# Performance work log

Measured on AMD Instinct MI355X. Metric: run time of the kernel, lower is better.

## Reference

```python
import jax, jax.numpy as jnp
import numpy as np

LOSS_WEIGHT = 20.0

def setup_inputs() -> dict:
    key = jax.random.key(0)
    ks = jax.random.split(key, 6)
    b, f, ns, nb, h, w = 8, 4, 7, 7, 128, 128
    # BCE input: keep strictly inside (0,1)
    segmentations = jax.random.uniform(ks[0], (b, f, nb, h, w), jnp.float32, 1e-4, 1.0 - 1e-4)
    masks = jax.random.uniform(ks[1], (b, f, ns, h, w), jnp.float32)
    reconstructions = jax.random.uniform(ks[2], (b, f, nb, 3, h, w), jnp.float32)
    rec_tgt = jax.random.uniform(ks[3], (b, f, 3, h, w), jnp.float32)
    masks_vis = jax.random.uniform(ks[4], (b, f, ns, h, w), jnp.float32)
    attn_index = jax.random.uniform(ks[5], (b, f, ns, nb), jnp.float32)
    return dict(segmentations=segmentations, masks=masks, reconstructions=reconstructions,
                rec_tgt=rec_tgt, masks_vis=masks_vis, attn_index=attn_index)

def reference(segmentations, masks, reconstructions, rec_tgt, masks_vis, attn_index):
    b, f, nb, h, w = segmentations.shape
    ns = masks.shape[2]
    N = b * f
    # broadcast instead of repeat: seg -> [N,1,nb,h,w], masks -> [N,ns,1,h,w]
    seg = segmentations.reshape(N, 1, nb, h, w)
    m = (masks.reshape(N, ns, 1, h, w) > 0.5).astype(seg.dtype)
    # torch BCE clamps log terms at -100
    logp = jnp.clip(jnp.log(seg), -100.0)
    log1mp = jnp.clip(jnp.log(1.0 - seg), -100.0)
    bce = -(m * logp + (1.0 - m) * log1mp)
    bce_term = jnp.sum(bce, axis=(-1, -2)) / (h * w)  # [N, ns, nb]
    # visibility mask broadcast over buffer and channel dims
    mv = (masks_vis.reshape(N, ns, 1, 1, h, w) > 0.5).astype(seg.dtype)
    rec_pred = reconstructions.reshape(N, 1, nb, 3, h, w) * mv   # [N,ns,nb,3,h,w]
    tgt = rec_tgt.reshape(N, 1, 1, 3, h, w) * mv
    mse_term = jnp.sum((rec_pred - tgt) ** 2, axis=(-3, -2, -1))  # [N, ns, nb]
    loss = bce_term + 0.1 * mse_term
    ai = attn_index.reshape(N, ns, nb)
    total = jnp.sum(ai * loss) / (b * f * ns * nb)
    return total * LOSS_WEIGHT
```

## Files before the change

kernel.cpp:

```cpp
#include <hip/hip_runtime.h>

#define HW 16384
#define NB 7
#define NS 7
#define NN 32

__global__ void zero_out_kernel(float* out) {
    if (threadIdx.x == 0 && blockIdx.x == 0) out[0] = 0.0f;
}

__global__ __launch_bounds__(256) void em_loss_kernel(
    const float* __restrict__ seg,
    const float* __restrict__ masks,
    const float* __restrict__ rec,
    const float* __restrict__ tgt,
    const float* __restrict__ mvis,
    const float* __restrict__ ai,
    float* __restrict__ out)
{
    const int n   = blockIdx.y;
    const int tid = threadIdx.x;
    const int pix = (blockIdx.x * blockDim.x + tid) * 4;

    __shared__ float s_ai[NS * NB];
    __shared__ float s_A[NB];
    __shared__ float s_part[4];

    if (tid < NS * NB) s_ai[tid] = ai[n * NS * NB + tid];
    __syncthreads();
    if (tid < NB) {
        float a = 0.0f;
        #pragma unroll
        for (int s = 0; s < NS; ++s) a += s_ai[s * NB + tid];
        s_A[tid] = a;
    }
    __syncthreads();

    const float* seg_n = seg   + (size_t)n * NB * HW + pix;
    const float* rec_n = rec   + (size_t)n * NB * 3 * HW + pix;
    const float* tgt_n = tgt   + (size_t)n * 3 * HW + pix;
    const float* msk_n = masks + (size_t)n * NS * HW + pix;
    const float* mv_n  = mvis  + (size_t)n * NS * HW + pix;

    float t[3][4];
    #pragma unroll
    for (int c = 0; c < 3; ++c) {
        float4 v = *reinterpret_cast<const float4*>(tgt_n + c * HW);
        t[c][0] = v.x; t[c][1] = v.y; t[c][2] = v.z; t[c][3] = v.w;
    }

    float d2[NB][4];
    #pragma unroll
    for (int b = 0; b < NB; ++b) {
        #pragma unroll
        for (int j = 0; j < 4; ++j) d2[b][j] = 0.0f;
        #pragma unroll
        for (int c = 0; c < 3; ++c) {
            float4 v = *reinterpret_cast<const float4*>(rec_n + (b * 3 + c) * HW);
            float r[4] = {v.x, v.y, v.z, v.w};
            #pragma unroll
            for (int j = 0; j < 4; ++j) {
                float d = r[j] - t[c][j];
                d2[b][j] += d * d;
            }
        }
    }

    float base[4] = {0.f, 0.f, 0.f, 0.f};
    float Ldiff[NB][4];
    #pragma unroll
    for (int b = 0; b < NB; ++b) {
        float4 v = *reinterpret_cast<const float4*>(seg_n + b * HW);
        float sv[4] = {v.x, v.y, v.z, v.w};
        float A = s_A[b];
        #pragma unroll
        for (int j = 0; j < 4; ++j) {
            float L1 = fminf(-__logf(sv[j]), 100.0f);
            float L0 = fminf(-__logf(1.0f - sv[j]), 100.0f);
            base[j] += A * L0;
            Ldiff[b][j] = L1 - L0;
        }
    }

    float bce[4] = {base[0], base[1], base[2], base[3]};
    float mse[4] = {0.f, 0.f, 0.f, 0.f};
    #pragma unroll
    for (int s = 0; s < NS; ++s) {
        float dotL[4] = {0.f, 0.f, 0.f, 0.f};
        float dotD[4] = {0.f, 0.f, 0.f, 0.f};
        #pragma unroll
        for (int b = 0; b < NB; ++b) {
            float a = s_ai[s * NB + b];
            #pragma unroll
            for (int j = 0; j < 4; ++j) {
                dotL[j] += a * Ldiff[b][j];
                dotD[j] += a * d2[b][j];
            }
        }
        float4 mk = *reinterpret_cast<const float4*>(msk_n + s * HW);
        float4 mv = *reinterpret_cast<const float4*>(mv_n + s * HW);
        float mkv[4] = {mk.x, mk.y, mk.z, mk.w};
        float mvv[4] = {mv.x, mv.y, mv.z, mv.w};
        #pragma unroll
        for (int j = 0; j < 4; ++j) {
            bce[j] += (mkv[j] > 0.5f) ? dotL[j] : 0.0f;
            mse[j] += (mvv[j] > 0.5f) ? dotD[j] : 0.0f;
        }
    }

    const float inv_hw = 1.0f / (float)HW;
    float acc = 0.0f;
    #pragma unroll
    for (int j = 0; j < 4; ++j) acc += bce[j] * inv_hw + 0.1f * mse[j];

    #pragma unroll
    for (int off = 32; off > 0; off >>= 1) acc += __shfl_down(acc, off, 64);

    const int wave = tid >> 6;
    const int lane = tid & 63;
    if (lane == 0) s_part[wave] = acc;
    __syncthreads();
    if (tid == 0) {
        float tsum = s_part[0] + s_part[1] + s_part[2] + s_part[3];
        atomicAdd(out, tsum * (20.0f / 1568.0f));
    }
}

extern "C" void kernel_launch(void* const* d_in, const int* in_sizes, int n_in,
                              void* d_out, int out_size, void* d_ws, size_t ws_size,
                              hipStream_t stream) {
    const float* seg  = (const float*)d_in[0];
    const float* msk  = (const float*)d_in[1];
    const float* rec  = (const float*)d_in[2];
    const float* tgt  = (const float*)d_in[3];
    const float* mvis = (const float*)d_in[4];
    const float* ai   = (const float*)d_in[5];
    float* out = (float*)d_out;

    zero_out_kernel<<<1, 64, 0, stream>>>(out);
    dim3 grid(HW / (256 * 4), NN);
    em_loss_kernel<<<grid, 256, 0, stream>>>(seg, msk, rec, tgt, mvis, ai, out);
}
```

Measured before the change: 123.6 us.

## Use one pixel per thread, precompute mask weights, and reduce partials without atomics

Each thread now handles one pixel with scalar loads instead of four pixels with float4, which gives four times as many blocks (2048) to hide memory latency. The per-pixel mask bits are folded into weight vectors over the buffer dimension, which lowers register pressure and avoids holding per-buffer intermediate arrays. The atomic accumulation and the zeroing kernel are replaced by per-block partials written to workspace, followed by a single-block reduction kernel. The cost is narrower loads and one more kernel launch, and the new path relies on the workspace being large enough for the partials.

```diff
diff --git a/kernel.cpp b/kernel.cpp
--- a/kernel.cpp
+++ b/kernel.cpp
@@ -4,23 +4,22 @@
 #define NB 7
 #define NS 7
 #define NN 32
+#define BLK 256
+#define GRIDX (HW / BLK)
+#define NPART (GRIDX * NN)
 
-__global__ void zero_out_kernel(float* out) {
-    if (threadIdx.x == 0 && blockIdx.x == 0) out[0] = 0.0f;
-}
-
-__global__ __launch_bounds__(256) void em_loss_kernel(
+__global__ __launch_bounds__(BLK, 4) void em_loss_main(
     const float* __restrict__ seg,
     const float* __restrict__ masks,
     const float* __restrict__ rec,
     const float* __restrict__ tgt,
     const float* __restrict__ mvis,
     const float* __restrict__ ai,
-    float* __restrict__ out)
+    float* __restrict__ partial)
 {
     const int n   = blockIdx.y;
     const int tid = threadIdx.x;
-    const int pix = (blockIdx.x * blockDim.x + tid) * 4;
+    const int pix = blockIdx.x * BLK + tid;
 
     __shared__ float s_ai[NS * NB];
     __shared__ float s_A[NB];
@@ -42,88 +41,75 @@
     const float* msk_n = masks + (size_t)n * NS * HW + pix;
     const float* mv_n  = mvis  + (size_t)n * NS * HW + pix;
 
-    float t[3][4];
+    float mkv[NS], mvv[NS];
     #pragma unroll
-    for (int c = 0; c < 3; ++c) {
-        float4 v = *reinterpret_cast<const float4*>(tgt_n + c * HW);
-        t[c][0] = v.x; t[c][1] = v.y; t[c][2] = v.z; t[c][3] = v.w;
-    }
+    for (int s = 0; s < NS; ++s) mkv[s] = msk_n[s * HW];
+    #pragma unroll
+    for (int s = 0; s < NS; ++s) mvv[s] = mv_n[s * HW];
 
-    float d2[NB][4];
+    float wl[NB], wd[NB];
     #pragma unroll
-    for (int b = 0; b < NB; ++b) {
+    for (int b = 0; b < NB; ++b) { wl[b] = 0.0f; wd[b] = 0.0f; }
+    #pragma unroll
+    for (int s = 0; s < NS; ++s) {
+        const float bm = (mkv[s] > 0.5f) ? 1.0f : 0.0f;
+        const float bv = (mvv[s] > 0.5f) ? 1.0f : 0.0f;
         #pragma unroll
-        for (int j = 0; j < 4; ++j) d2[b][j] = 0.0f;
-        #pragma unroll
-        for (int c = 0; c < 3; ++c) {
-            float4 v = *reinterpret_cast<const float4*>(rec_n + (b * 3 + c) * HW);
-            float r[4] = {v.x, v.y, v.z, v.w};
-            #pragma unroll
-            for (int j = 0; j < 4; ++j) {
-                float d = r[j] - t[c][j];
-                d2[b][j] += d * d;
-            }
+        for (int b = 0; b < NB; ++b) {
+            const float a = s_ai[s * NB + b];
+            wl[b] += bm * a;
+            wd[b] += bv * a;
         }
     }
 
-    float base[4] = {0.f, 0.f, 0.f, 0.f};
-    float Ldiff[NB][4];
+    const float t0 = tgt_n[0];
+    const float t1 = tgt_n[HW];
+    const float t2 = tgt_n[2 * HW];
+
+    float acc_bce = 0.0f, acc_mse = 0.0f;
     #pragma unroll
     for (int b = 0; b < NB; ++b) {
-        float4 v = *reinterpret_cast<const float4*>(seg_n + b * HW);
-        float sv[4] = {v.x, v.y, v.z, v.w};
-        float A = s_A[b];
-        #pragma unroll
-        for (int j = 0; j < 4; ++j) {
-            float L1 = fminf(-__logf(sv[j]), 100.0f);
-            float L0 = fminf(-__logf(1.0f - sv[j]), 100.0f);
-            base[j] += A * L0;
-            Ldiff[b][j] = L1 - L0;
-        }
+        const float sv = seg_n[b * HW];
+        const float r0 = rec_n[(b * 3 + 0) * HW];
+        const float r1 = rec_n[(b * 3 + 1) * HW];
+        const float r2 = rec_n[(b * 3 + 2) * HW];
+        const float L1 = fminf(-__logf(sv), 100.0f);
+        const float L0 = fminf(-__logf(1.0f - sv), 100.0f);
+        acc_bce += s_A[b] * L0 + wl[b] * (L1 - L0);
+        const float d0 = r0 - t0, d1 = r1 - t1, d2 = r2 - t2;
+        acc_mse += wd[b] * (d0 * d0 + d1 * d1 + d2 * d2);
     }
 
-    float bce[4] = {base[0], base[1], base[2], base[3]};
-    float mse[4] = {0.f, 0.f, 0.f, 0.f};
-    #pragma unroll
-    for (int s = 0; s < NS; ++s) {
-        float dotL[4] = {0.f, 0.f, 0.f, 0.f};
-        float dotD[4] = {0.f, 0.f, 0.f, 0.f};
-        #pragma unroll
-        for (int b = 0; b < NB; ++b) {
-            float a = s_ai[s * NB + b];
-            #pragma unroll
-            for (int j = 0; j < 4; ++j) {
-                dotL[j] += a * Ldiff[b][j];
-                dotD[j] += a * d2[b][j];
-            }
-        }
-        float4 mk = *reinterpret_cast<const float4*>(msk_n + s * HW);
-        float4 mv = *reinterpret_cast<const float4*>(mv_n + s * HW);
-        float mkv[4] = {mk.x, mk.y, mk.z, mk.w};
-        float mvv[4] = {mv.x, mv.y, mv.z, mv.w};
-        #pragma unroll
-        for (int j = 0; j < 4; ++j) {
-            bce[j] += (mkv[j] > 0.5f) ? dotL[j] : 0.0f;
-            mse[j] += (mvv[j] > 0.5f) ? dotD[j] : 0.0f;
-        }
-    }
-
-    const float inv_hw = 1.0f / (float)HW;
-    float acc = 0.0f;
-    #pragma unroll
-    for (int j = 0; j < 4; ++j) acc += bce[j] * inv_hw + 0.1f * mse[j];
+    float acc = acc_bce * (1.0f / (float)HW) + 0.1f * acc_mse;
 
     #pragma unroll
     for (int off = 32; off > 0; off >>= 1) acc += __shfl_down(acc, off, 64);
-
     const int wave = tid >> 6;
     const int lane = tid & 63;
     if (lane == 0) s_part[wave] = acc;
     __syncthreads();
     if (tid == 0) {
-        float tsum = s_part[0] + s_part[1] + s_part[2] + s_part[3];
-        atomicAdd(out, tsum * (20.0f / 1568.0f));
+        partial[blockIdx.y * GRIDX + blockIdx.x] =
+            s_part[0] + s_part[1] + s_part[2] + s_part[3];
     }
+}
+
+__global__ __launch_bounds__(BLK) void em_loss_reduce(
+    const float* __restrict__ partial, float* __restrict__ out)
+{
+    __shared__ float s_part[4];
+    const int tid = threadIdx.x;
+    float a = 0.0f;
+    #pragma unroll
+    for (int i = 0; i < NPART / BLK; ++i) a += partial[i * BLK + tid];
+    #pragma unroll
+    for (int off = 32; off > 0; off >>= 1) a += __shfl_down(a, off, 64);
+    const int wave = tid >> 6;
+    const int lane = tid & 63;
+    if (lane == 0) s_part[wave] = a;
+    __syncthreads();
+    if (tid == 0)
+        out[0] = (s_part[0] + s_part[1] + s_part[2] + s_part[3]) * (20.0f / 1568.0f);
 }
 
 extern "C" void kernel_launch(void* const* d_in, const int* in_sizes, int n_in,
@@ -135,9 +121,10 @@
     const float* tgt  = (const float*)d_in[3];
     const float* mvis = (const float*)d_in[4];
     const float* ai   = (const float*)d_in[5];
-    float* out = (float*)d_out;
+    float* out     = (float*)d_out;
+    float* partial = (float*)d_ws;
 
-    zero_out_kernel<<<1, 64, 0, stream>>>(out);
-    dim3 grid(HW / (256 * 4), NN);
-    em_loss_kernel<<<grid, 256, 0, stream>>>(seg, msk, rec, tgt, mvis, ai, out);
+    dim3 grid(GRIDX, NN);
+    em_loss_main<<<grid, BLK, 0, stream>>>(seg, msk, rec, tgt, mvis, ai, partial);
+    em_loss_reduce<<<1, BLK, 0, stream>>>(partial, out);
 }
```

After: 115.8 us. 6.3% less time.
